# Kernel tuning notes

Hardware: AMD Instinct MI355X
Metric: run time of the kernel (lower is better)

The kernel has to match this reference:

```python
import jax, jax.numpy as jnp
import numpy as np

B, L, D, V, C = 128, 128, 512, 50000, 512  # batch, leaves, embed_dim, vocab, num_category
NODES = 2 * L - 1


def setup_inputs() -> dict:
    key = jax.random.key(0)
    k1, k2, k3, k4 = jax.random.split(key, 4)
    leaf_content_id = jax.random.randint(k1, (B, L), 0, V)
    # leaves occupy positions 0..L-1; internal nodes fill L..2L-2 during compose
    content_mask = jnp.concatenate(
        [jnp.ones((B, L), dtype=bool), jnp.zeros((B, L - 1), dtype=bool)], axis=1)
    # each step composes two already-available nodes; leaf indices are always valid
    composition_info = jax.random.randint(k2, (B, L - 1, 2), 0, L)
    emb_weight = jax.random.normal(k3, (V, D), dtype=jnp.float32) * 0.02
    lin_w = jax.random.normal(k4, (C, D), dtype=jnp.float32) * 0.02
    lin_b = jnp.zeros((C,), dtype=jnp.float32)
    return dict(leaf_content_id=leaf_content_id, content_mask=content_mask,
                composition_info=composition_info, emb_weight=emb_weight,
                lin_w=lin_w, lin_b=lin_b)


def circular_correlation(a, b):
    # corr(a, b) = irfft(conj(rfft(a)) * rfft(b))
    fa = jnp.fft.rfft(a, axis=-1)
    fb = jnp.fft.rfft(b, axis=-1)
    return jnp.fft.irfft(jnp.conj(fa) * fb, n=a.shape[-1], axis=-1)


def reference(leaf_content_id, content_mask, composition_info, emb_weight, lin_w, lin_b):
    Bq, Lq = leaf_content_id.shape
    nodes = 2 * Lq - 1
    Dq = emb_weight.shape[1]
    # embed leaves into positions where content_mask is True (first L slots)
    leaf_vec = emb_weight[leaf_content_id]                      # [B, L, D]
    vector = jnp.zeros((Bq, nodes, Dq), dtype=emb_weight.dtype)
    vector = vector.at[:, :Lq].set(jnp.where(content_mask[:, :Lq, None], leaf_vec, 0.0))
    batch_ar = jnp.arange(Bq)

    def step(vec, xs):
        idx, li, ri = xs                                        # li, ri: [B]
        left = vec[batch_ar, li]                                # gather [B, D]
        right = vec[batch_ar, ri]
        comp = circular_correlation(left, right)                # [B, D]
        # internal node for step idx lands at position L + idx (rolled mask)
        vec = jax.lax.dynamic_update_slice(vec, comp[:, None, :], (0, Lq + idx, 0))
        return vec, None

    xs = (jnp.arange(Lq - 1),
          composition_info[:, :, 0].T.astype(jnp.int32),
          composition_info[:, :, 1].T.astype(jnp.int32))
    vector, _ = jax.lax.scan(step, vector, xs)
    logits = jnp.einsum('bnd,cd->bnc', vector, lin_w) + lin_b   # [B, 2L-1, C]
    return jax.nn.sigmoid(logits)
```

## Files before the change

### kernel.cpp

```cpp
#include <hip/hip_runtime.h>
#include <hip/hip_bf16.h>

#define Bq 128
#define Lq 128
#define Dq 512
#define NODES 255
#define Cq 512
#define M_ROWS (Bq * NODES)
#define FP8_SCALE 64.0f
#define INV_SCALE2 (1.0f / (FP8_SCALE * FP8_SCALE))

typedef unsigned int uint32;
typedef unsigned char uchar;
typedef _Float16 v8hf __attribute__((ext_vector_type(8)));
typedef __fp16 v2fp __attribute__((ext_vector_type(2)));
typedef float v4f __attribute__((ext_vector_type(4)));
typedef unsigned int v4u __attribute__((ext_vector_type(4)));

typedef __attribute__((address_space(3))) void lds_void_t;
typedef const __attribute__((address_space(1))) void gbl_void_t;

__device__ inline uint32 packh(float lo, float hi) {
    v2fp p = __builtin_amdgcn_cvt_pkrtz(lo, hi);
    return __builtin_bit_cast(uint32, p);
}
__device__ inline uint32 fp8x4(float a, float b, float c, float d) {
    int lo = __builtin_amdgcn_cvt_pk_fp8_f32(a, b, 0, false);
    return (uint32)__builtin_amdgcn_cvt_pk_fp8_f32(c, d, lo, true);
}
__device__ inline uchar fp8b(float a) {
    return (uchar)(__builtin_amdgcn_cvt_pk_fp8_f32(a, a, 0, false) & 0xFF);
}

#define CW 1552

__global__ __launch_bounds__(256) void prep_kernel(const int* __restrict__ ids,
                                                   const int* __restrict__ cinfo,
                                                   const float* __restrict__ emb,
                                                   const float* __restrict__ linw,
                                                   uchar* __restrict__ nodev,
                                                   uchar* __restrict__ wb) {
    __shared__ __align__(16) uint32 lds[4 * CW];
    int bid = blockIdx.x;
    int wave = threadIdx.x >> 6, lane = threadIdx.x & 63;

    if (bid < 4096) {
        int b = bid >> 5;
        int idx = (bid & 31) * 4 + wave;
        idx = idx < Lq - 1 ? idx : Lq - 2;
        int li = cinfo[(b * (Lq - 1) + idx) * 2 + 0];
        int ri = cinfo[(b * (Lq - 1) + idx) * 2 + 1];
        int lid = ids[b * Lq + li];
        int rid = ids[b * Lq + ri];
        uint32* W = lds + wave * CW;

        const float4* lr = (const float4*)(emb + (size_t)lid * Dq);
        const float4* rr = (const float4*)(emb + (size_t)rid * Dq);
        float4 a0 = lr[2 * lane], a1 = lr[2 * lane + 1];
        float4 c0 = rr[2 * lane], c1 = rr[2 * lane + 1];
        v4u ua = {packh(a0.x, a0.y), packh(a0.z, a0.w), packh(a1.x, a1.y), packh(a1.z, a1.w)};
        v4u ub = {packh(c0.x, c0.y), packh(c0.z, c0.w), packh(c1.x, c1.y), packh(c1.z, c1.w)};
        ((v4u*)(W))[lane] = ua;
        ((v4u*)(W + 256))[lane] = ua;
        ((v4u*)(W + 512))[lane] = ub;
        ((v4u*)(W + 768))[lane] = ub;
        uint32 dn = (uint32)__shfl((int)ub.x, (lane + 1) & 63);
        v4u uo;
        uo.x = __builtin_amdgcn_alignbit(ub.y, ub.x, 16);
        uo.y = __builtin_amdgcn_alignbit(ub.z, ub.y, 16);
        uo.z = __builtin_amdgcn_alignbit(ub.w, ub.z, 16);
        uo.w = __builtin_amdgcn_alignbit(dn,   ub.w, 16);
        ((v4u*)(W + 1028))[lane] = uo;
        ((v4u*)(W + 1284))[lane] = uo;

        int m = lane & 15, q = lane >> 4;
        const uint32* A0 = W + (4 * q - 8 * m + 256);
        const uint32* A1 = W + (4 * q - 8 * m + 128);
        const uint32* PB = W + ((lane & 1) ? 1028 : 512) + 4 * q + ((lane & 15) >> 1);
        v4f acc0 = {0.f, 0.f, 0.f, 0.f};
        v4f acc1 = {0.f, 0.f, 0.f, 0.f};
#pragma unroll
        for (int kb = 0; kb < 16; ++kb) {
            v4u Ra = *((const v4u*)(A0 + 16 * kb));
            v4u Rb = *((const v4u*)(A1 + 16 * kb));
            v4u RB;
            RB.x = PB[16 * kb + 0]; RB.y = PB[16 * kb + 1];
            RB.z = PB[16 * kb + 2]; RB.w = PB[16 * kb + 3];
            v8hf fa0 = __builtin_bit_cast(v8hf, Ra);
            v8hf fa1 = __builtin_bit_cast(v8hf, Rb);
            v8hf fb  = __builtin_bit_cast(v8hf, RB);
            acc0 = __builtin_amdgcn_mfma_f32_16x16x32_f16(fa0, fb, acc0, 0, 0, 0);
            acc1 = __builtin_amdgcn_mfma_f32_16x16x32_f16(fa1, fb, acc1, 0, 0, 0);
        }

        uchar* orow = nodev + ((size_t)b * NODES + Lq + idx) * Dq;
        int n = lane & 15;
#pragma unroll
        for (int r = 0; r < 4; ++r) {
            orow[16 * (4 * q + r) + n]       = fp8b(acc0[r] * FP8_SCALE);
            orow[256 + 16 * (4 * q + r) + n] = fp8b(acc1[r] * FP8_SCALE);
        }
    } else if (bid < 8192) {
        int r = (bid - 4096) * 4 + wave;
        int b = r >> 7, l = r & (Lq - 1);
        int id = ids[r];
        int e = lane * 8;
        const float* src = emb + (size_t)id * Dq + e;
        float4 v0 = *((const float4*)src);
        float4 v1 = *((const float4*)(src + 4));
        uint2 o;
        o.x = fp8x4(v0.x * FP8_SCALE, v0.y * FP8_SCALE, v0.z * FP8_SCALE, v0.w * FP8_SCALE);
        o.y = fp8x4(v1.x * FP8_SCALE, v1.y * FP8_SCALE, v1.z * FP8_SCALE, v1.w * FP8_SCALE);
        *((uint2*)(nodev + ((size_t)b * NODES + l) * Dq + e)) = o;
    } else {
        int i = ((bid - 8192) * 256 + threadIdx.x) * 8;
        float4 v0 = *((const float4*)(linw + i));
        float4 v1 = *((const float4*)(linw + i + 4));
        uint2 o;
        o.x = fp8x4(v0.x * FP8_SCALE, v0.y * FP8_SCALE, v0.z * FP8_SCALE, v0.w * FP8_SCALE);
        o.y = fp8x4(v1.x * FP8_SCALE, v1.y * FP8_SCALE, v1.z * FP8_SCALE, v1.w * FP8_SCALE);
        *((uint2*)(wb + i)) = o;
    }
}

__global__ __launch_bounds__(256) void gemm_kernel(const uchar* __restrict__ Vm,
                                                   const uchar* __restrict__ Wm,
                                                   const float* __restrict__ bias,
                                                   float* __restrict__ out) {
    __shared__ __align__(16) uchar Wt[128 * 32];
    __shared__ __align__(16) uchar Vt[128 * 32];
    int t = threadIdx.x;
    int colBase = blockIdx.x * 128;
    int rowBase = blockIdx.y * 128;
    int wave = t >> 6, lane = t & 63;
    int q = lane & 15, quad = lane >> 4;
    int wc = (wave & 1) * 64;
    int wv = (wave >> 1) * 64;

    v4f acc[4][4];
#pragma unroll
    for (int i = 0; i < 4; ++i)
#pragma unroll
        for (int j = 0; j < 4; ++j)
            acc[i][j] = (v4f){0.f, 0.f, 0.f, 0.f};

    const uchar* gW = Wm + (size_t)(colBase + (t >> 1)) * Dq + (t & 1) * 16;
    const uchar* gV = Vm + (size_t)(rowBase + (t >> 1)) * Dq + (t & 1) * 16;
    uchar* lW = Wt + t * 16;
    uchar* lV = Vt + t * 16;

    for (int k0 = 0; k0 < Dq; k0 += 32) {
        __syncthreads();
        __builtin_amdgcn_global_load_lds((gbl_void_t*)(gW + k0), (lds_void_t*)lW, 16, 0, 0);
        __builtin_amdgcn_global_load_lds((gbl_void_t*)(gV + k0), (lds_void_t*)lV, 16, 0, 0);
        __syncthreads();

        long wf[4], vf[4];
#pragma unroll
        for (int i = 0; i < 4; ++i)
            wf[i] = *((const long*)(Wt + (wc + i * 16 + q) * 32 + quad * 8));
#pragma unroll
        for (int j = 0; j < 4; ++j)
            vf[j] = *((const long*)(Vt + (wv + j * 16 + q) * 32 + quad * 8));
#pragma unroll
        for (int i = 0; i < 4; ++i)
#pragma unroll
            for (int j = 0; j < 4; ++j)
                acc[i][j] = __builtin_amdgcn_mfma_f32_16x16x32_fp8_fp8(wf[i], vf[j], acc[i][j], 0, 0, 0);
    }

#pragma unroll
    for (int i = 0; i < 4; ++i) {
        int cb = colBase + wc + i * 16 + quad * 4;
        float4 b4 = *((const float4*)(bias + cb));
#pragma unroll
        for (int j = 0; j < 4; ++j) {
            int grow = rowBase + wv + j * 16 + q;
            float4 o4;
            o4.x = 1.f / (1.f + __expf(-(acc[i][j][0] * INV_SCALE2 + b4.x)));
            o4.y = 1.f / (1.f + __expf(-(acc[i][j][1] * INV_SCALE2 + b4.y)));
            o4.z = 1.f / (1.f + __expf(-(acc[i][j][2] * INV_SCALE2 + b4.z)));
            o4.w = 1.f / (1.f + __expf(-(acc[i][j][3] * INV_SCALE2 + b4.w)));
            *((float4*)(out + (size_t)grow * Cq + cb)) = o4;
        }
    }
}

extern "C" void kernel_launch(void* const* d_in, const int* in_sizes, int n_in,
                              void* d_out, int out_size, void* d_ws, size_t ws_size,
                              hipStream_t stream) {
    const int*   ids   = (const int*)d_in[0];
    const int*   cinfo = (const int*)d_in[2];
    const float* emb   = (const float*)d_in[3];
    const float* linw  = (const float*)d_in[4];
    const float* linb  = (const float*)d_in[5];
    float* out = (float*)d_out;

    uchar* nodev = (uchar*)d_ws;
    uchar* wb = nodev + (size_t)M_ROWS * Dq;

    prep_kernel<<<dim3(8320), dim3(256), 0, stream>>>(ids, cinfo, emb, linw, nodev, wb);
    gemm_kernel<<<dim3(Cq / 128, M_ROWS / 128), dim3(256), 0, stream>>>(nodev, wb, linb, out);

    (void)in_sizes; (void)n_in; (void)out_size; (void)ws_size;
}
```

Measured before the change: 215.3 us.

## Double-buffer GEMM LDS tiles with K=64 stages and XOR-swizzled layout

The fp8 GEMM kernel now uses two LDS buffers and takes K in steps of 64 instead of 32. Each step issues the global-to-LDS loads for the next tile before running the MFMAs on the current one, which halves the number of barriers. A 16-byte-chunk XOR swizzle is applied on both the store and the read side to cut LDS bank conflicts. In exchange, LDS use per block grows fourfold, which may lower occupancy. There is also no explicit vmcnt wait before the barrier, so correctness depends on the barrier waiting for outstanding loads.

```diff
diff --git a/kernel.cpp b/kernel.cpp
--- a/kernel.cpp
+++ b/kernel.cpp
@@ -127,13 +127,14 @@
                                                    const uchar* __restrict__ Wm,
                                                    const float* __restrict__ bias,
                                                    float* __restrict__ out) {
-    __shared__ __align__(16) uchar Wt[128 * 32];
-    __shared__ __align__(16) uchar Vt[128 * 32];
+    __shared__ __align__(16) uchar Wt[2][128 * 64];
+    __shared__ __align__(16) uchar Vt[2][128 * 64];
     int t = threadIdx.x;
     int colBase = blockIdx.x * 128;
     int rowBase = blockIdx.y * 128;
     int wave = t >> 6, lane = t & 63;
     int q = lane & 15, quad = lane >> 4;
+    int qhi = quad >> 1, qlo = quad & 1;
     int wc = (wave & 1) * 64;
     int wv = (wave >> 1) * 64;
 
@@ -144,30 +145,50 @@
         for (int j = 0; j < 4; ++j)
             acc[i][j] = (v4f){0.f, 0.f, 0.f, 0.f};
 
-    const uchar* gW = Wm + (size_t)(colBase + (t >> 1)) * Dq + (t & 1) * 16;
-    const uchar* gV = Vm + (size_t)(rowBase + (t >> 1)) * Dq + (t & 1) * 16;
-    uchar* lW = Wt + t * 16;
-    uchar* lV = Vt + t * 16;
-
-    for (int k0 = 0; k0 < Dq; k0 += 32) {
+    int rowA = t >> 2;
+    int src = ((t & 3) ^ (rowA & 3)) << 4;
+    const uchar* gWA = Wm + (size_t)(colBase + rowA) * Dq + src;
+    const uchar* gWB = Wm + (size_t)(colBase + 64 + rowA) * Dq + src;
+    const uchar* gVA = Vm + (size_t)(rowBase + rowA) * Dq + src;
+    const uchar* gVB = Vm + (size_t)(rowBase + 64 + rowA) * Dq + src;
+    int dA = t * 16;
+    int dB = 4096 + t * 16;
+
+#define STAGE(B, K0) do { \
+    __builtin_amdgcn_global_load_lds((gbl_void_t*)(gWA + (K0)), (lds_void_t*)(&Wt[B][dA]), 16, 0, 0); \
+    __builtin_amdgcn_global_load_lds((gbl_void_t*)(gWB + (K0)), (lds_void_t*)(&Wt[B][dB]), 16, 0, 0); \
+    __builtin_amdgcn_global_load_lds((gbl_void_t*)(gVA + (K0)), (lds_void_t*)(&Vt[B][dA]), 16, 0, 0); \
+    __builtin_amdgcn_global_load_lds((gbl_void_t*)(gVB + (K0)), (lds_void_t*)(&Vt[B][dB]), 16, 0, 0); \
+  } while (0)
+
+    STAGE(0, 0);
+    __syncthreads();
+
+#pragma unroll
+    for (int ks = 0; ks < 8; ++ks) {
+        int buf = ks & 1;
+        if (ks < 7) STAGE(buf ^ 1, (ks + 1) * 64);
+        const uchar* Wb = Wt[buf];
+        const uchar* Vb = Vt[buf];
+#pragma unroll
+        for (int kk = 0; kk < 2; ++kk) {
+            int off = ((((kk << 1) | qhi) ^ (q & 3)) << 4) | (qlo << 3);
+            long wf[4], vf[4];
+#pragma unroll
+            for (int i = 0; i < 4; ++i)
+                wf[i] = *((const long*)(Wb + (wc + i * 16 + q) * 64 + off));
+#pragma unroll
+            for (int j = 0; j < 4; ++j)
+                vf[j] = *((const long*)(Vb + (wv + j * 16 + q) * 64 + off));
+#pragma unroll
+            for (int i = 0; i < 4; ++i)
+#pragma unroll
+                for (int j = 0; j < 4; ++j)
+                    acc[i][j] = __builtin_amdgcn_mfma_f32_16x16x32_fp8_fp8(wf[i], vf[j], acc[i][j], 0, 0, 0);
+        }
         __syncthreads();
-        __builtin_amdgcn_global_load_lds((gbl_void_t*)(gW + k0), (lds_void_t*)lW, 16, 0, 0);
-        __builtin_amdgcn_global_load_lds((gbl_void_t*)(gV + k0), (lds_void_t*)lV, 16, 0, 0);
-        __syncthreads();
-
-        long wf[4], vf[4];
-#pragma unroll
-        for (int i = 0; i < 4; ++i)
-            wf[i] = *((const long*)(Wt + (wc + i * 16 + q) * 32 + quad * 8));
-#pragma unroll
-        for (int j = 0; j < 4; ++j)
-            vf[j] = *((const long*)(Vt + (wv + j * 16 + q) * 32 + quad * 8));
-#pragma unroll
-        for (int i = 0; i < 4; ++i)
-#pragma unroll
-            for (int j = 0; j < 4; ++j)
-                acc[i][j] = __builtin_amdgcn_mfma_f32_16x16x32_fp8_fp8(wf[i], vf[j], acc[i][j], 0, 0, 0);
     }
+#undef STAGE
 
 #pragma unroll
     for (int i = 0; i < 4; ++i) {
```

After: 214.8 us. About the same (-0.3%).

## Fuse node construction into GEMM, keeping 64-row node tiles in swizzled LDS

Applied to the files above, without the earlier changes.

Replaces the separate prep kernel and GEMM with one fused kernel. Each 512-thread block builds 64 node rows (leaf embeddings or circular correlations via MFMA) directly into XOR-swizzled shared memory, then multiplies them against all 512 columns of the fp8 weight, which each wave streams from global memory into registers with a one-step prefetch. This removes the global write and re-read of the fp8 node matrix and one kernel launch. In exchange, each block redoes the weight reads with no LDS sharing, the LDS footprint is larger, which may limit occupancy, and the correlation work is spread unevenly across waves.

```diff
diff --git a/kernel.cpp b/kernel.cpp
--- a/kernel.cpp
+++ b/kernel.cpp
@@ -17,9 +17,6 @@
 typedef float v4f __attribute__((ext_vector_type(4)));
 typedef unsigned int v4u __attribute__((ext_vector_type(4)));
 
-typedef __attribute__((address_space(3))) void lds_void_t;
-typedef const __attribute__((address_space(1))) void gbl_void_t;
-
 __device__ inline uint32 packh(float lo, float hi) {
     v2fp p = __builtin_amdgcn_cvt_pkrtz(lo, hi);
     return __builtin_bit_cast(uint32, p);
@@ -32,110 +29,118 @@
     return (uchar)(__builtin_amdgcn_cvt_pk_fp8_f32(a, a, 0, false) & 0xFF);
 }
 
-#define CW 1552
-
-__global__ __launch_bounds__(256) void prep_kernel(const int* __restrict__ ids,
-                                                   const int* __restrict__ cinfo,
-                                                   const float* __restrict__ emb,
-                                                   const float* __restrict__ linw,
-                                                   uchar* __restrict__ nodev,
-                                                   uchar* __restrict__ wb) {
-    __shared__ __align__(16) uint32 lds[4 * CW];
-    int bid = blockIdx.x;
-    int wave = threadIdx.x >> 6, lane = threadIdx.x & 63;
-
-    if (bid < 4096) {
-        int b = bid >> 5;
-        int idx = (bid & 31) * 4 + wave;
-        idx = idx < Lq - 1 ? idx : Lq - 2;
-        int li = cinfo[(b * (Lq - 1) + idx) * 2 + 0];
-        int ri = cinfo[(b * (Lq - 1) + idx) * 2 + 1];
-        int lid = ids[b * Lq + li];
-        int rid = ids[b * Lq + ri];
-        uint32* W = lds + wave * CW;
-
-        const float4* lr = (const float4*)(emb + (size_t)lid * Dq);
-        const float4* rr = (const float4*)(emb + (size_t)rid * Dq);
-        float4 a0 = lr[2 * lane], a1 = lr[2 * lane + 1];
-        float4 c0 = rr[2 * lane], c1 = rr[2 * lane + 1];
-        v4u ua = {packh(a0.x, a0.y), packh(a0.z, a0.w), packh(a1.x, a1.y), packh(a1.z, a1.w)};
-        v4u ub = {packh(c0.x, c0.y), packh(c0.z, c0.w), packh(c1.x, c1.y), packh(c1.z, c1.w)};
-        ((v4u*)(W))[lane] = ua;
-        ((v4u*)(W + 256))[lane] = ua;
-        ((v4u*)(W + 512))[lane] = ub;
-        ((v4u*)(W + 768))[lane] = ub;
-        uint32 dn = (uint32)__shfl((int)ub.x, (lane + 1) & 63);
-        v4u uo;
-        uo.x = __builtin_amdgcn_alignbit(ub.y, ub.x, 16);
-        uo.y = __builtin_amdgcn_alignbit(ub.z, ub.y, 16);
-        uo.z = __builtin_amdgcn_alignbit(ub.w, ub.z, 16);
-        uo.w = __builtin_amdgcn_alignbit(dn,   ub.w, 16);
-        ((v4u*)(W + 1028))[lane] = uo;
-        ((v4u*)(W + 1284))[lane] = uo;
-
-        int m = lane & 15, q = lane >> 4;
-        const uint32* A0 = W + (4 * q - 8 * m + 256);
-        const uint32* A1 = W + (4 * q - 8 * m + 128);
-        const uint32* PB = W + ((lane & 1) ? 1028 : 512) + 4 * q + ((lane & 15) >> 1);
-        v4f acc0 = {0.f, 0.f, 0.f, 0.f};
-        v4f acc1 = {0.f, 0.f, 0.f, 0.f};
-#pragma unroll
-        for (int kb = 0; kb < 16; ++kb) {
-            v4u Ra = *((const v4u*)(A0 + 16 * kb));
-            v4u Rb = *((const v4u*)(A1 + 16 * kb));
-            v4u RB;
-            RB.x = PB[16 * kb + 0]; RB.y = PB[16 * kb + 1];
-            RB.z = PB[16 * kb + 2]; RB.w = PB[16 * kb + 3];
-            v8hf fa0 = __builtin_bit_cast(v8hf, Ra);
-            v8hf fa1 = __builtin_bit_cast(v8hf, Rb);
-            v8hf fb  = __builtin_bit_cast(v8hf, RB);
-            acc0 = __builtin_amdgcn_mfma_f32_16x16x32_f16(fa0, fb, acc0, 0, 0, 0);
-            acc1 = __builtin_amdgcn_mfma_f32_16x16x32_f16(fa1, fb, acc1, 0, 0, 0);
-        }
-
-        uchar* orow = nodev + ((size_t)b * NODES + Lq + idx) * Dq;
-        int n = lane & 15;
-#pragma unroll
-        for (int r = 0; r < 4; ++r) {
-            orow[16 * (4 * q + r) + n]       = fp8b(acc0[r] * FP8_SCALE);
-            orow[256 + 16 * (4 * q + r) + n] = fp8b(acc1[r] * FP8_SCALE);
-        }
-    } else if (bid < 8192) {
-        int r = (bid - 4096) * 4 + wave;
-        int b = r >> 7, l = r & (Lq - 1);
-        int id = ids[r];
-        int e = lane * 8;
-        const float* src = emb + (size_t)id * Dq + e;
-        float4 v0 = *((const float4*)src);
-        float4 v1 = *((const float4*)(src + 4));
-        uint2 o;
-        o.x = fp8x4(v0.x * FP8_SCALE, v0.y * FP8_SCALE, v0.z * FP8_SCALE, v0.w * FP8_SCALE);
-        o.y = fp8x4(v1.x * FP8_SCALE, v1.y * FP8_SCALE, v1.z * FP8_SCALE, v1.w * FP8_SCALE);
-        *((uint2*)(nodev + ((size_t)b * NODES + l) * Dq + e)) = o;
-    } else {
-        int i = ((bid - 8192) * 256 + threadIdx.x) * 8;
-        float4 v0 = *((const float4*)(linw + i));
-        float4 v1 = *((const float4*)(linw + i + 4));
-        uint2 o;
-        o.x = fp8x4(v0.x * FP8_SCALE, v0.y * FP8_SCALE, v0.z * FP8_SCALE, v0.w * FP8_SCALE);
-        o.y = fp8x4(v1.x * FP8_SCALE, v1.y * FP8_SCALE, v1.z * FP8_SCALE, v1.w * FP8_SCALE);
-        *((uint2*)(wb + i)) = o;
+__global__ __launch_bounds__(256) void wconv_kernel(const float* __restrict__ linw,
+                                                    uchar* __restrict__ wb) {
+    int i = (blockIdx.x * 256 + threadIdx.x) * 8;
+    float4 v0 = *((const float4*)(linw + i));
+    float4 v1 = *((const float4*)(linw + i + 4));
+    uint2 o;
+    o.x = fp8x4(v0.x * FP8_SCALE, v0.y * FP8_SCALE, v0.z * FP8_SCALE, v0.w * FP8_SCALE);
+    o.y = fp8x4(v1.x * FP8_SCALE, v1.y * FP8_SCALE, v1.z * FP8_SCALE, v1.w * FP8_SCALE);
+    *((uint2*)(wb + i)) = o;
+}
+
+#define CW2 1296
+
+__global__ __launch_bounds__(512, 4) void fused_kernel(const int* __restrict__ ids,
+                                                       const int* __restrict__ cinfo,
+                                                       const float* __restrict__ emb,
+                                                       const uchar* __restrict__ wb,
+                                                       const float* __restrict__ bias,
+                                                       float* __restrict__ out) {
+    __shared__ __align__(16) uchar smem[32768 + CW2 * 4 * 8];
+    uchar* Vt = smem;
+    uint32* scratch = (uint32*)(smem + 32768);
+    int t = threadIdx.x;
+    int wave = t >> 6, lane = t & 63;
+    int blk = blockIdx.x;
+
+    uint32* W = scratch + wave * CW2;
+    int q = lane >> 4, m = lane & 15;
+#pragma unroll
+    for (int ri = 0; ri < 8; ++ri) {
+        int r = ri * 8 + wave;
+        int R = blk * 64 + r;
+        int b = R / 255;
+        int node = R - b * 255;
+        int key = (r & 7) << 4;
+        uchar* vrow = Vt + r * 512;
+        if (node < Lq) {
+            int id = ids[b * Lq + node];
+            const float* src = emb + (size_t)id * Dq + lane * 8;
+            float4 v0 = *((const float4*)src);
+            float4 v1 = *((const float4*)(src + 4));
+            uint2 o;
+            o.x = fp8x4(v0.x * FP8_SCALE, v0.y * FP8_SCALE, v0.z * FP8_SCALE, v0.w * FP8_SCALE);
+            o.y = fp8x4(v1.x * FP8_SCALE, v1.y * FP8_SCALE, v1.z * FP8_SCALE, v1.w * FP8_SCALE);
+            int byte = (((lane >> 1) << 4) ^ key) | ((lane & 1) << 3);
+            *((uint2*)(vrow + byte)) = o;
+        } else {
+            int idx = node - Lq;
+            int li = cinfo[(b * (Lq - 1) + idx) * 2 + 0];
+            int rx = cinfo[(b * (Lq - 1) + idx) * 2 + 1];
+            int lid = ids[b * Lq + li];
+            int rid = ids[b * Lq + rx];
+            const float4* lr = (const float4*)(emb + (size_t)lid * Dq);
+            const float4* rr = (const float4*)(emb + (size_t)rid * Dq);
+            float4 a0 = lr[2 * lane], a1 = lr[2 * lane + 1];
+            float4 c0 = rr[2 * lane], c1 = rr[2 * lane + 1];
+            v4u ua = {packh(a0.x, a0.y), packh(a0.z, a0.w), packh(a1.x, a1.y), packh(a1.z, a1.w)};
+            v4u ub = {packh(c0.x, c0.y), packh(c0.z, c0.w), packh(c1.x, c1.y), packh(c1.z, c1.w)};
+            ((v4u*)(W))[lane] = ua;
+            ((v4u*)(W + 256))[lane] = ua;
+            ((v4u*)(W + 512))[lane] = ub;
+            ((v4u*)(W + 768))[lane] = ub;
+            uint32 dn = (uint32)__shfl((int)ub.x, (lane + 1) & 63);
+            v4u uo;
+            uo.x = __builtin_amdgcn_alignbit(ub.y, ub.x, 16);
+            uo.y = __builtin_amdgcn_alignbit(ub.z, ub.y, 16);
+            uo.z = __builtin_amdgcn_alignbit(ub.w, ub.z, 16);
+            uo.w = __builtin_amdgcn_alignbit(dn,   ub.w, 16);
+            ((v4u*)(W + 1028))[lane] = uo;
+            if (lane < 2) ((v4u*)(W + 1284))[lane] = uo;
+
+            const uint32* A0 = W + (4 * q - 8 * m + 256);
+            const uint32* A1 = W + (4 * q - 8 * m + 128);
+            const uint32* PB = W + ((lane & 1) ? 1028 : 512) + 4 * q + (m >> 1);
+            v4f acc0 = {0.f, 0.f, 0.f, 0.f};
+            v4f acc1 = {0.f, 0.f, 0.f, 0.f};
+#pragma unroll
+            for (int kb = 0; kb < 16; ++kb) {
+                v4u Ra = *((const v4u*)(A0 + 16 * kb));
+                v4u Rb = *((const v4u*)(A1 + 16 * kb));
+                v4u RB;
+                RB.x = PB[16 * kb + 0]; RB.y = PB[16 * kb + 1];
+                RB.z = PB[16 * kb + 2]; RB.w = PB[16 * kb + 3];
+                v8hf fa0 = __builtin_bit_cast(v8hf, Ra);
+                v8hf fa1 = __builtin_bit_cast(v8hf, Rb);
+                v8hf fb  = __builtin_bit_cast(v8hf, RB);
+                acc0 = __builtin_amdgcn_mfma_f32_16x16x32_f16(fa0, fb, acc0, 0, 0, 0);
+                acc1 = __builtin_amdgcn_mfma_f32_16x16x32_f16(fa1, fb, acc1, 0, 0, 0);
+            }
+#pragma unroll
+            for (int rr2 = 0; rr2 < 4; ++rr2) {
+                int ch = 4 * q + rr2;
+                vrow[(((ch)      << 4) ^ key) | m] = fp8b(acc0[rr2] * FP8_SCALE);
+                vrow[(((ch + 16) << 4) ^ key) | m] = fp8b(acc1[rr2] * FP8_SCALE);
+            }
+        }
     }
-}
-
-__global__ __launch_bounds__(256) void gemm_kernel(const uchar* __restrict__ Vm,
-                                                   const uchar* __restrict__ Wm,
-                                                   const float* __restrict__ bias,
-                                                   float* __restrict__ out) {
-    __shared__ __align__(16) uchar Wt[128 * 32];
-    __shared__ __align__(16) uchar Vt[128 * 32];
-    int t = threadIdx.x;
-    int colBase = blockIdx.x * 128;
-    int rowBase = blockIdx.y * 128;
-    int wave = t >> 6, lane = t & 63;
-    int q = lane & 15, quad = lane >> 4;
-    int wc = (wave & 1) * 64;
-    int wv = (wave >> 1) * 64;
+
+    int quad = lane >> 4, qq = lane & 15;
+    int qhi = quad >> 1, qlo = quad & 1;
+    int cw = wave * 64;
+
+    const uchar* wp[4];
+#pragma unroll
+    for (int i = 0; i < 4; ++i)
+        wp[i] = wb + (size_t)(cw + 16 * i + qq) * Dq + 8 * quad;
+    long wreg[4];
+#pragma unroll
+    for (int i = 0; i < 4; ++i)
+        wreg[i] = *((const long*)(wp[i]));
+
+    __syncthreads();
 
     v4f acc[4][4];
 #pragma unroll
@@ -144,38 +149,37 @@
         for (int j = 0; j < 4; ++j)
             acc[i][j] = (v4f){0.f, 0.f, 0.f, 0.f};
 
-    const uchar* gW = Wm + (size_t)(colBase + (t >> 1)) * Dq + (t & 1) * 16;
-    const uchar* gV = Vm + (size_t)(rowBase + (t >> 1)) * Dq + (t & 1) * 16;
-    uchar* lW = Wt + t * 16;
-    uchar* lV = Vt + t * 16;
-
-    for (int k0 = 0; k0 < Dq; k0 += 32) {
-        __syncthreads();
-        __builtin_amdgcn_global_load_lds((gbl_void_t*)(gW + k0), (lds_void_t*)lW, 16, 0, 0);
-        __builtin_amdgcn_global_load_lds((gbl_void_t*)(gV + k0), (lds_void_t*)lV, 16, 0, 0);
-        __syncthreads();
-
-        long wf[4], vf[4];
+#pragma unroll
+    for (int ks = 0; ks < 16; ++ks) {
+        long wcur[4];
+#pragma unroll
+        for (int i = 0; i < 4; ++i) wcur[i] = wreg[i];
+        if (ks < 15) {
+#pragma unroll
+            for (int i = 0; i < 4; ++i)
+                wreg[i] = *((const long*)(wp[i] + 32 * (ks + 1)));
+        }
+        long vf[4];
+#pragma unroll
+        for (int j = 0; j < 4; ++j) {
+            int row = 16 * j + qq;
+            int phys = (2 * ks + qhi) ^ (qq & 7);
+            vf[j] = *((const long*)(Vt + row * 512 + phys * 16 + qlo * 8));
+        }
 #pragma unroll
         for (int i = 0; i < 4; ++i)
-            wf[i] = *((const long*)(Wt + (wc + i * 16 + q) * 32 + quad * 8));
-#pragma unroll
-        for (int j = 0; j < 4; ++j)
-            vf[j] = *((const long*)(Vt + (wv + j * 16 + q) * 32 + quad * 8));
-#pragma unroll
-        for (int i = 0; i < 4; ++i)
 #pragma unroll
             for (int j = 0; j < 4; ++j)
-                acc[i][j] = __builtin_amdgcn_mfma_f32_16x16x32_fp8_fp8(wf[i], vf[j], acc[i][j], 0, 0, 0);
+                acc[i][j] = __builtin_amdgcn_mfma_f32_16x16x32_fp8_fp8(wcur[i], vf[j], acc[i][j], 0, 0, 0);
     }
 
 #pragma unroll
     for (int i = 0; i < 4; ++i) {
-        int cb = colBase + wc + i * 16 + quad * 4;
+        int cb = cw + 16 * i + 4 * quad;
         float4 b4 = *((const float4*)(bias + cb));
 #pragma unroll
         for (int j = 0; j < 4; ++j) {
-            int grow = rowBase + wv + j * 16 + q;
+            int grow = blk * 64 + 16 * j + qq;
             float4 o4;
             o4.x = 1.f / (1.f + __expf(-(acc[i][j][0] * INV_SCALE2 + b4.x)));
             o4.y = 1.f / (1.f + __expf(-(acc[i][j][1] * INV_SCALE2 + b4.y)));
@@ -196,11 +200,10 @@
     const float* linb  = (const float*)d_in[5];
     float* out = (float*)d_out;
 
-    uchar* nodev = (uchar*)d_ws;
-    uchar* wb = nodev + (size_t)M_ROWS * Dq;
-
-    prep_kernel<<<dim3(8320), dim3(256), 0, stream>>>(ids, cinfo, emb, linw, nodev, wb);
-    gemm_kernel<<<dim3(Cq / 128, M_ROWS / 128), dim3(256), 0, stream>>>(nodev, wb, linb, out);
+    uchar* wb = (uchar*)d_ws;
+
+    wconv_kernel<<<dim3(128), dim3(256), 0, stream>>>(linw, wb);
+    fused_kernel<<<dim3(M_ROWS / 64), dim3(512), 0, stream>>>(ids, cinfo, emb, wb, linb, out);
 
     (void)in_sizes; (void)n_in; (void)out_size; (void)ws_size;
 }
```

Result: no change. 214.5 us (-0.4%).
